# Performance work log

Hardware: AMD Instinct MI355X
Metric: run time of the kernel (lower is better)

## Reference

```python
import jax, jax.numpy as jnp
import numpy as np

B, T, I, H = 32, 2048, 256, 256
LN_EPS = 1e-5


def _lstm_dir(x, Wih, Whh, b):
    """Single-direction LSTM. x: [B,T,I]; Wih: [4H,I]; Whh: [4H,H]; b: [4H].
    PyTorch gate order: i, f, g, o. Returns hidden sequence [B,T,H]."""
    # Precompute input projection for all timesteps (one big GEMM).
    xW = jnp.einsum('bti,gi->btg', x, Wih) + b  # [B,T,4H]
    xW = jnp.swapaxes(xW, 0, 1)                 # [T,B,4H] for scan
    h0 = jnp.zeros((x.shape[0], Whh.shape[1]), x.dtype)
    c0 = jnp.zeros_like(h0)

    def step(carry, xt):
        h, c = carry
        gates = xt + h @ Whh.T                  # [B,4H]
        i, f, g, o = jnp.split(gates, 4, axis=-1)
        i = jax.nn.sigmoid(i)
        f = jax.nn.sigmoid(f)
        g = jnp.tanh(g)
        o = jax.nn.sigmoid(o)
        c = f * c + i * g
        h = o * jnp.tanh(c)
        return (h, c), h

    _, hs = jax.lax.scan(step, (h0, c0), xW)
    return jnp.swapaxes(hs, 0, 1)               # [B,T,H]


def _forward(x, Wih_f, Whh_f, b_f, Wih_b, Whh_b, b_b, ln_g, ln_b, fc_W, fc_b):
    h_fwd = _lstm_dir(x, Wih_f, Whh_f, b_f)
    h_bwd = _lstm_dir(x[:, ::-1, :], Wih_b, Whh_b, b_b)[:, ::-1, :]
    h = jnp.concatenate([h_fwd, h_bwd], axis=-1)     # [B,T,2H]
    # LayerNorm over last dim
    mu = jnp.mean(h, axis=-1, keepdims=True)
    var = jnp.mean((h - mu) ** 2, axis=-1, keepdims=True)
    h = (h - mu) * jax.lax.rsqrt(var + LN_EPS) * ln_g + ln_b
    # Linear 2H -> H (bidirectional branch). Dropout is identity in eval mode.
    return jnp.einsum('btk,hk->bth', h, fc_W) + fc_b


def setup_inputs() -> dict:
    key = jax.random.key(0)
    ks = jax.random.split(key, 10)
    s = 1.0 / np.sqrt(H)
    return {
        'x': jax.random.normal(ks[0], (B, T, I), jnp.float32),
        'Wih_f': jax.random.uniform(ks[1], (4 * H, I), jnp.float32, -s, s),
        'Whh_f': jax.random.uniform(ks[2], (4 * H, H), jnp.float32, -s, s),
        'b_f': jax.random.uniform(ks[3], (4 * H,), jnp.float32, -s, s),
        'Wih_b': jax.random.uniform(ks[4], (4 * H, I), jnp.float32, -s, s),
        'Whh_b': jax.random.uniform(ks[5], (4 * H, H), jnp.float32, -s, s),
        'b_b': jax.random.uniform(ks[6], (4 * H,), jnp.float32, -s, s),
        'ln_g': jnp.ones((2 * H,), jnp.float32),
        'ln_b': jnp.zeros((2 * H,), jnp.float32),
        'fc_W': jax.random.uniform(ks[7], (H, 2 * H), jnp.float32, -s, s),
        'fc_b': jax.random.uniform(ks[8], (H,), jnp.float32, -s, s),
    }


def reference(x, Wih_f, Whh_f, b_f, Wih_b, Whh_b, b_b, ln_g, ln_b, fc_W, fc_b):
    return _forward(x, Wih_f, Whh_f, b_f, Wih_b, Whh_b, b_b, ln_g, ln_b, fc_W, fc_b)
```

## Files before the change

kernel.cpp:

```cpp
#include <hip/hip_runtime.h>
#include <cstdint>
#include <cstddef>

#define BDIM 32
#define TDIM 2048
#define IDIM 256
#define HDIM 256
#define CHUNK 128
#define NCHUNK (TDIM / CHUNK)
#define GEMM_WGS 512

using short8 = __attribute__((ext_vector_type(8))) short;
using f32x4  = __attribute__((ext_vector_type(4))) float;
typedef _Float16 half2v __attribute__((ext_vector_type(2)));

__device__ __forceinline__ float bflo(uint32_t u) { return __uint_as_float(u << 16); }
__device__ __forceinline__ float bfhi(uint32_t u) { return __uint_as_float(u & 0xffff0000u); }
__device__ __forceinline__ uint16_t f2bf(float f) {
  uint32_t u = __float_as_uint(f);
  uint32_t r = u + 0x7fffu + ((u >> 16) & 1u);
  return (uint16_t)(r >> 16);
}
__device__ __forceinline__ uint16_t f2h_bits(float f) {
  _Float16 h = (_Float16)f;
  return __builtin_bit_cast(uint16_t, h);
}
__device__ __forceinline__ float h2f(uint16_t b) {
  return (float)__builtin_bit_cast(_Float16, b);
}
__device__ __forceinline__ half2v as_h2(uint32_t u) {
  return __builtin_bit_cast(half2v, u);
}
__device__ __forceinline__ float h2lo(uint32_t u) { return (float)as_h2(u)[0]; }
__device__ __forceinline__ float h2hi(uint32_t u) { return (float)as_h2(u)[1]; }

#if __has_builtin(__builtin_amdgcn_fdot2)
__device__ __forceinline__ float DOT2(half2v a, half2v b, float c) {
  return __builtin_amdgcn_fdot2(a, b, c, false);
}
#else
__device__ __forceinline__ float DOT2(half2v a, half2v b, float c) {
  return c + (float)a[0] * (float)b[0] + (float)a[1] * (float)b[1];
}
#endif

__device__ __forceinline__ float sigmoidf_fast(float x) {
  return 1.f / (1.f + __expf(-x));
}
__device__ __forceinline__ float tanhf_fast(float x) {
  float a = fabsf(x);
  float e = __expf(2.f * a);
  float t = 1.f - 2.f / (e + 1.f);
  return copysignf(t, x);
}


__global__ void k_cvt4(const float* __restrict__ src, uint16_t* __restrict__ dst, int n4) {
  int i = blockIdx.x * blockDim.x + threadIdx.x;
  if (i >= n4) return;
  const float4 v = ((const float4*)src)[i];
  ushort4 o;
  o.x = f2bf(v.x); o.y = f2bf(v.y); o.z = f2bf(v.z); o.w = f2bf(v.w);
  ((ushort4*)dst)[i] = o;
}

__global__ void k_zero(float* __restrict__ p, int n) {
  int i = blockIdx.x * blockDim.x + threadIdx.x;
  if (i < n) p[i] = 0.f;
}

__global__ void k_build_wcat(const float* __restrict__ wf, const float* __restrict__ wb,
                             const float* __restrict__ biasf, const float* __restrict__ biasb,
                             uint16_t* __restrict__ wcat, float* __restrict__ biasp) {
  int id = blockIdx.x * 256 + threadIdx.x;
  int k = id & 255;
  int j = id >> 8;
  int dir = j >> 10;
  int jj = j & 1023;
  int n = jj >> 2;
  int g = jj & 3;
  const float* W = dir ? wb : wf;
  wcat[id] = f2bf(W[(g * 256 + n) * 256 + k]);
  if (k == 0) biasp[j] = (dir ? biasb : biasf)[g * 256 + n];
}

__global__ void k_build_wrec2(const float* __restrict__ whf, const float* __restrict__ whb,
                              uint16_t* __restrict__ wrec2) {
  int id = blockIdx.x * 256 + threadIdx.x;
  int j  = id & 1;
  int g  = (id >> 1) & 3;
  int n  = (id >> 3) & 255;
  int kp = (id >> 11) & 127;
  int dir = (id >> 18) & 1;
  const float* W = dir ? whb : whf;
  wrec2[id] = f2h_bits(W[(g * 256 + n) * 256 + 2 * kp + j]);
}

__global__ __launch_bounds__(1024) void k_fused(
    const float* __restrict__ x,
    const uint16_t* __restrict__ wcat,
    const float* __restrict__ biasp,
    uint16_t* __restrict__ xw_prod,
    const uint16_t* __restrict__ xw_cons,
    const uint16_t* __restrict__ wrec2,
    uint16_t* __restrict__ hcat,
    float* __restrict__ hstate,
    float* __restrict__ cstate,
    int c0, int c0g, int do_lstm, int do_gemm) {
  const int tid = threadIdx.x;

  if (blockIdx.x < 64) {
    if (!do_lstm) return;
    __shared__ uint16_t hhalf[256];
    __shared__ float part[4][256][4];

    const int w = blockIdx.x;
    const int b = w >> 1;
    const int dir = w & 1;
    const int n = tid & 255;
    const int q = tid >> 8;

    const uint16_t* wbase = wrec2 + ((size_t)(dir * 128 + q * 32) * 256 + n) * 8;

    float c = 0.f, hlast = 0.f;
    if (tid < 256) {
      hlast = hstate[w * 256 + tid];
      c = cstate[w * 256 + tid];
      hhalf[tid] = f2h_bits(hlast);
    }
    __syncthreads();

    for (int sl = 0; sl < CHUNK; ++sl) {
      const int t = dir ? (TDIM - 1 - (c0 + sl)) : (c0 + sl);

      uint2 xv;
      if (tid < 256)
        xv = *(const uint2*)(xw_cons + ((size_t)(sl * 32 + b)) * 2048 + dir * 1024 + tid * 4);

      float ai = 0.f, af = 0.f, ag = 0.f, ao = 0.f;
      const uint16_t* wp = wbase;
#pragma unroll 8
      for (int it = 0; it < 32; ++it) {
        const half2v hp = as_h2(*(const uint32_t*)&hhalf[2 * (q * 32 + it)]);
        const uint4 wv = *(const uint4*)wp;
        wp += 2048;
        ai = DOT2(as_h2(wv.x), hp, ai);
        af = DOT2(as_h2(wv.y), hp, af);
        ag = DOT2(as_h2(wv.z), hp, ag);
        ao = DOT2(as_h2(wv.w), hp, ao);
      }
      f32x4 pv; pv[0] = ai; pv[1] = af; pv[2] = ag; pv[3] = ao;
      *(f32x4*)(&part[q][n][0]) = pv;
      __syncthreads();

      if (tid < 256) {
        const f32x4 p0 = *(const f32x4*)(&part[0][tid][0]);
        const f32x4 p1 = *(const f32x4*)(&part[1][tid][0]);
        const f32x4 p2 = *(const f32x4*)(&part[2][tid][0]);
        const f32x4 p3 = *(const f32x4*)(&part[3][tid][0]);
        float gi = p0[0] + p1[0] + p2[0] + p3[0] + h2lo(xv.x);
        float gf = p0[1] + p1[1] + p2[1] + p3[1] + h2hi(xv.x);
        float gg = p0[2] + p1[2] + p2[2] + p3[2] + h2lo(xv.y);
        float go = p0[3] + p1[3] + p2[3] + p3[3] + h2hi(xv.y);
        const float I = sigmoidf_fast(gi);
        const float F = sigmoidf_fast(gf);
        const float G = tanhf_fast(gg);
        const float O = sigmoidf_fast(go);
        c = F * c + I * G;
        const float h = O * tanhf_fast(c);
        hlast = h;
        const uint16_t hb = f2h_bits(h);
        hhalf[tid] = hb;
        hcat[((size_t)(b * TDIM + t)) * 512 + dir * 256 + tid] = hb;
      }
      __syncthreads();
    }

    if (tid < 256) {
      hstate[w * 256 + tid] = hlast;
      cstate[w * 256 + tid] = c;
    }
    return;
  }

  if (!do_gemm) return;
  const int gb = blockIdx.x - 64;
  const int mt = gb >> 4;
  const int nt = gb & 15;
  const int dir = nt >> 3;
  const int wv_ = tid >> 6;
  const int wm = wv_ & 3;
  const int wn = wv_ >> 2;
  const int lane = tid & 63;
  const int l15 = lane & 15;
  const int lg  = lane >> 4;

  const float* Abase[2];
  int colg[2];
  const uint16_t* Bbase[2];
  float bv[2], fvv[2];
#pragma unroll
  for (int mi = 0; mi < 2; ++mi) {
    const int row = mt * 128 + wm * 32 + mi * 16 + l15;
    const int s_local = row >> 5;
    const int b = row & 31;
    const int t = dir ? (TDIM - 1 - (c0g + s_local)) : (c0g + s_local);
    Abase[mi] = x + ((size_t)(b * TDIM + t)) * 256 + lg * 8;
  }
#pragma unroll
  for (int ni = 0; ni < 2; ++ni) {
    colg[ni] = nt * 128 + wn * 32 + ni * 16 + l15;
    Bbase[ni] = wcat + (size_t)colg[ni] * 256 + lg * 8;
    bv[ni] = biasp[colg[ni]];
    (void)fvv;
  }

  f32x4 acc[2][2] = {};
#pragma unroll
  for (int ks = 0; ks < 8; ++ks) {
    short8 a[2];
#pragma unroll
    for (int mi = 0; mi < 2; ++mi) {
      const float4 f0 = *(const float4*)(Abase[mi] + ks * 32);
      const float4 f1 = *(const float4*)(Abase[mi] + ks * 32 + 4);
      a[mi][0] = (short)f2bf(f0.x); a[mi][1] = (short)f2bf(f0.y);
      a[mi][2] = (short)f2bf(f0.z); a[mi][3] = (short)f2bf(f0.w);
      a[mi][4] = (short)f2bf(f1.x); a[mi][5] = (short)f2bf(f1.y);
      a[mi][6] = (short)f2bf(f1.z); a[mi][7] = (short)f2bf(f1.w);
    }
#pragma unroll
    for (int ni = 0; ni < 2; ++ni) {
      const short8 bfr = *(const short8*)(Bbase[ni] + ks * 32);
#pragma unroll
      for (int mi = 0; mi < 2; ++mi)
        acc[mi][ni] = __builtin_amdgcn_mfma_f32_16x16x32_bf16(a[mi], bfr, acc[mi][ni], 0, 0, 0);
    }
  }

#pragma unroll
  for (int mi = 0; mi < 2; ++mi)
#pragma unroll
    for (int ni = 0; ni < 2; ++ni)
#pragma unroll
      for (int r = 0; r < 4; ++r) {
        const int row = mt * 128 + wm * 32 + mi * 16 + lg * 4 + r;
        xw_prod[(size_t)row * 2048 + colg[ni]] = f2h_bits(acc[mi][ni][r] + bv[ni]);
      }
}

__global__ __launch_bounds__(256) void k_lnfc2(
    const uint16_t* __restrict__ hcat,
    const float* __restrict__ lng, const float* __restrict__ lnb,
    const uint16_t* __restrict__ fcwb,
    const float* __restrict__ fcb,
    float* __restrict__ out) {
  __shared__ uint16_t lnh[64 * 520];
  __shared__ float slng[512], slnb[512];

  const int tid = threadIdx.x;
  const size_t bt0 = (size_t)blockIdx.x * 64;

  slng[tid] = lng[tid]; slng[tid + 256] = lng[tid + 256];
  slnb[tid] = lnb[tid]; slnb[tid + 256] = lnb[tid + 256];

  const int row = tid >> 2;
  const int part = tid & 3;
  const uint16_t* hrow = hcat + (bt0 + row) * 512;
  float s = 0.f, s2 = 0.f;
#pragma unroll
  for (int i = 0; i < 16; ++i) {
    const uint4 u = *(const uint4*)(hrow + (i * 4 + part) * 8);
    const float f0 = h2lo(u.x), f1 = h2hi(u.x), f2 = h2lo(u.y), f3 = h2hi(u.y);
    const float f4 = h2lo(u.z), f5 = h2hi(u.z), f6 = h2lo(u.w), f7 = h2hi(u.w);
    s  += ((f0 + f1) + (f2 + f3)) + ((f4 + f5) + (f6 + f7));
    s2 += ((f0*f0 + f1*f1) + (f2*f2 + f3*f3)) + ((f4*f4 + f5*f5) + (f6*f6 + f7*f7));
  }
  s  += __shfl_xor(s, 1, 64);  s  += __shfl_xor(s, 2, 64);
  s2 += __shfl_xor(s2, 1, 64); s2 += __shfl_xor(s2, 2, 64);
  const float mu = s * (1.f / 512.f);
  const float var = s2 * (1.f / 512.f) - mu * mu;
  const float rs = rsqrtf(var + 1e-5f);
  __syncthreads();

#pragma unroll
  for (int i = 0; i < 16; ++i) {
    const int kb = (i * 4 + part) * 8;
    const uint4 u = *(const uint4*)(hrow + kb);
    uint16_t tmp[8] __attribute__((aligned(16)));
    const float f[8] = { h2lo(u.x), h2hi(u.x), h2lo(u.y), h2hi(u.y),
                         h2lo(u.z), h2hi(u.z), h2lo(u.w), h2hi(u.w) };
#pragma unroll
    for (int e = 0; e < 8; ++e)
      tmp[e] = f2bf((f[e] - mu) * rs * slng[kb + e] + slnb[kb + e]);
    *(short8*)&lnh[row * 520 + kb] = *(const short8*)tmp;
  }
  __syncthreads();

  const int w = tid >> 6;
  const int lane = tid & 63;
  const int l15 = lane & 15;
  const int lg = lane >> 4;
  f32x4 acc[4][4] = {};
#pragma unroll
  for (int nf = 0; nf < 4; ++nf) {
    const uint16_t* bb = fcwb + (size_t)(w * 64 + nf * 16 + l15) * 512 + lg * 8;
#pragma unroll 4
    for (int k0 = 0; k0 < 16; ++k0) {
      const short8 bfr = *(const short8*)(bb + k0 * 32);
#pragma unroll
      for (int mf = 0; mf < 4; ++mf) {
        const short8 afr = *(const short8*)&lnh[(mf * 16 + l15) * 520 + k0 * 32 + lg * 8];
        acc[mf][nf] = __builtin_amdgcn_mfma_f32_16x16x32_bf16(afr, bfr, acc[mf][nf], 0, 0, 0);
      }
    }
  }
#pragma unroll
  for (int nf = 0; nf < 4; ++nf) {
    const int col = w * 64 + nf * 16 + l15;
    const float fv = fcb[col];
#pragma unroll
    for (int mf = 0; mf < 4; ++mf)
#pragma unroll
      for (int r = 0; r < 4; ++r)
        out[(bt0 + mf * 16 + lg * 4 + r) * 256 + col] = acc[mf][nf][r] + fv;
  }
}


extern "C" void kernel_launch(void* const* d_in, const int* in_sizes, int n_in,
                              void* d_out, int out_size, void* d_ws, size_t ws_size,
                              hipStream_t stream) {
  const float* x    = (const float*)d_in[0];
  const float* Wihf = (const float*)d_in[1];
  const float* Whhf = (const float*)d_in[2];
  const float* bf_  = (const float*)d_in[3];
  const float* Wihb = (const float*)d_in[4];
  const float* Whhb = (const float*)d_in[5];
  const float* bb_  = (const float*)d_in[6];
  const float* lng  = (const float*)d_in[7];
  const float* lnb  = (const float*)d_in[8];
  const float* fcW  = (const float*)d_in[9];
  const float* fcb  = (const float*)d_in[10];
  float* out = (float*)d_out;

  char* ws = (char*)d_ws;
  size_t off = 0;
  uint16_t* wcat  = (uint16_t*)(ws + off); off += (size_t)2048 * 256 * 2;
  float*    biasp = (float*)(ws + off);    off += (size_t)2048 * 4;
  uint16_t* wrec2 = (uint16_t*)(ws + off); off += (size_t)2 * 128 * 256 * 8 * 2;
  uint16_t* fcwb  = (uint16_t*)(ws + off); off += (size_t)256 * 512 * 2;
  float*    hstate= (float*)(ws + off);    off += (size_t)64 * 256 * 4;
  float*    cstate= (float*)(ws + off);    off += (size_t)64 * 256 * 4;
  uint16_t* xw0   = (uint16_t*)(ws + off); off += (size_t)(CHUNK * 32) * 2048 * 2;
  uint16_t* xw1   = (uint16_t*)(ws + off); off += (size_t)(CHUNK * 32) * 2048 * 2;
  uint16_t* hcat  = (uint16_t*)(ws + off); off += (size_t)65536 * 512 * 2;
  (void)ws_size; (void)in_sizes; (void)n_in; (void)out_size;

  k_cvt4<<<128, 256, 0, stream>>>(fcW, fcwb, 131072 / 4);
  k_build_wcat<<<2048, 256, 0, stream>>>(Wihf, Wihb, bf_, bb_, wcat, biasp);
  k_build_wrec2<<<2048, 256, 0, stream>>>(Whhf, Whhb, wrec2);
  k_zero<<<128, 256, 0, stream>>>(hstate, 64 * 256 * 2);

  k_fused<<<64 + GEMM_WGS, 1024, 0, stream>>>(x, wcat, biasp, xw0, xw1, wrec2,
                                              hcat, hstate, cstate, 0, 0, 0, 1);

  for (int ck = 0; ck < NCHUNK; ++ck) {
    uint16_t* cons = (ck & 1) ? xw1 : xw0;
    uint16_t* prod = (ck & 1) ? xw0 : xw1;
    const int dg = (ck < NCHUNK - 1) ? 1 : 0;
    const int grid = 64 + (dg ? GEMM_WGS : 0);
    k_fused<<<grid, 1024, 0, stream>>>(x, wcat, biasp, prod, cons, wrec2,
                                       hcat, hstate, cstate,
                                       ck * CHUNK, (ck + 1) * CHUNK, 1, dg);
  }

  k_lnfc2<<<1024, 256, 0, stream>>>(hcat, lng, lnb, fcwb, fcb, out);
}
```

Baseline: 8.640 ms.

## Replace chunked LSTM launches with persistent cross-block kernel using register-resident weights

```diff
diff --git a/kernel.cpp b/kernel.cpp
--- a/kernel.cpp
+++ b/kernel.cpp
@@ -8,14 +8,11 @@
 #define HDIM 256
 #define CHUNK 128
 #define NCHUNK (TDIM / CHUNK)
-#define GEMM_WGS 512
 
 using short8 = __attribute__((ext_vector_type(8))) short;
 using f32x4  = __attribute__((ext_vector_type(4))) float;
 typedef _Float16 half2v __attribute__((ext_vector_type(2)));
 
-__device__ __forceinline__ float bflo(uint32_t u) { return __uint_as_float(u << 16); }
-__device__ __forceinline__ float bfhi(uint32_t u) { return __uint_as_float(u & 0xffff0000u); }
 __device__ __forceinline__ uint16_t f2bf(float f) {
   uint32_t u = __float_as_uint(f);
   uint32_t r = u + 0x7fffu + ((u >> 16) & 1u);
@@ -24,9 +21,6 @@
 __device__ __forceinline__ uint16_t f2h_bits(float f) {
   _Float16 h = (_Float16)f;
   return __builtin_bit_cast(uint16_t, h);
-}
-__device__ __forceinline__ float h2f(uint16_t b) {
-  return (float)__builtin_bit_cast(_Float16, b);
 }
 __device__ __forceinline__ half2v as_h2(uint32_t u) {
   return __builtin_bit_cast(half2v, u);
@@ -64,9 +58,9 @@
   ((ushort4*)dst)[i] = o;
 }
 
-__global__ void k_zero(float* __restrict__ p, int n) {
+__global__ void k_zero_u32(uint32_t* __restrict__ p, int n) {
   int i = blockIdx.x * blockDim.x + threadIdx.x;
-  if (i < n) p[i] = 0.f;
+  if (i < n) p[i] = 0u;
 }
 
 __global__ void k_build_wcat(const float* __restrict__ wf, const float* __restrict__ wb,
@@ -84,168 +78,191 @@
   if (k == 0) biasp[j] = (dir ? biasb : biasf)[g * 256 + n];
 }
 
-__global__ void k_build_wrec2(const float* __restrict__ whf, const float* __restrict__ whb,
-                              uint16_t* __restrict__ wrec2) {
+__global__ void k_build_wrec3(const float* __restrict__ whf, const float* __restrict__ whb,
+                              uint32_t* __restrict__ wrec3) {
   int id = blockIdx.x * 256 + threadIdx.x;
-  int j  = id & 1;
-  int g  = (id >> 1) & 3;
-  int n  = (id >> 3) & 255;
-  int kp = (id >> 11) & 127;
-  int dir = (id >> 18) & 1;
+  int g   = id & 3;
+  int n   = (id >> 2) & 63;
+  int j   = (id >> 8) & 15;
+  int kq  = (id >> 12) & 7;
+  int qq  = (id >> 15) & 3;
+  int dir = (id >> 17) & 1;
   const float* W = dir ? whb : whf;
-  wrec2[id] = f2h_bits(W[(g * 256 + n) * 256 + 2 * kp + j]);
-}
-
-__global__ __launch_bounds__(1024) void k_fused(
+  const int row = g * 256 + qq * 64 + n;
+  const int k0  = kq * 32 + 2 * j;
+  const uint32_t lo = f2h_bits(W[row * 256 + k0]);
+  const uint32_t hi = f2h_bits(W[row * 256 + k0 + 1]);
+  const int oidx = ((((dir * 4 + qq) * 8 + kq) * 16 + j) * 64 + n) * 4 + g;
+  wrec3[oidx] = lo | (hi << 16);
+}
+
+__global__ __launch_bounds__(512, 2) void k_lstm_persist(
     const float* __restrict__ x,
     const uint16_t* __restrict__ wcat,
     const float* __restrict__ biasp,
-    uint16_t* __restrict__ xw_prod,
-    const uint16_t* __restrict__ xw_cons,
-    const uint16_t* __restrict__ wrec2,
-    uint16_t* __restrict__ hcat,
-    float* __restrict__ hstate,
-    float* __restrict__ cstate,
-    int c0, int c0g, int do_lstm, int do_gemm) {
-  const int tid = threadIdx.x;
-
-  if (blockIdx.x < 64) {
-    if (!do_lstm) return;
-    __shared__ uint16_t hhalf[256];
-    __shared__ float part[4][256][4];
-
-    const int w = blockIdx.x;
-    const int b = w >> 1;
-    const int dir = w & 1;
-    const int n = tid & 255;
-    const int q = tid >> 8;
-
-    const uint16_t* wbase = wrec2 + ((size_t)(dir * 128 + q * 32) * 256 + n) * 8;
-
-    float c = 0.f, hlast = 0.f;
-    if (tid < 256) {
-      hlast = hstate[w * 256 + tid];
-      c = cstate[w * 256 + tid];
-      hhalf[tid] = f2h_bits(hlast);
+    const uint32_t* __restrict__ wrec3,
+    uint16_t* __restrict__ xwp_all,
+    uint32_t* __restrict__ hcat32,
+    uint32_t* __restrict__ cnt) {
+  __shared__ uint4 ldsbig[84 * 1024 / 16];
+  f32x4*    partsh = (f32x4*)ldsbig;
+  uint32_t* h2lds  = (uint32_t*)(ldsbig + 448);
+
+  const int bid  = blockIdx.x;
+  const int pair = bid & 63;
+  const int q    = bid >> 6;
+  const int b    = pair >> 1;
+  const int dir  = pair & 1;
+  const int tid  = threadIdx.x;
+  const int kq   = tid >> 6;
+  const int lane = tid & 63;
+
+  uint4 wr[16];
+  {
+    const uint4* wsrc = (const uint4*)wrec3 + ((((dir * 4 + q) * 8 + kq) * 16) * 64 + lane);
+#pragma unroll
+    for (int j = 0; j < 16; ++j) wr[j] = wsrc[j * 64];
+  }
+
+  if (tid < 128) h2lds[tid] = 0u;
+  float creg = 0.f;
+  __syncthreads();
+
+  uint16_t* xwp = xwp_all + (size_t)bid * (2 * CHUNK * 256);
+  const int l15 = lane & 15;
+  const int lg  = lane >> 4;
+  const int colbase = dir * 1024 + q * 256;
+  const uint32_t cmy = pair * 4 + q;
+
+  auto gemm_chunk = [&](int ck) {
+    const int p = ck & 1;
+    const int sl0 = kq * 16;
+    const int slA = sl0 + l15;
+    const int tA = dir ? (TDIM - 1 - (ck * CHUNK + slA)) : (ck * CHUNK + slA);
+    const float* Abase = x + ((size_t)(b * TDIM + tA)) * 256 + lg * 8;
+    uint16_t* xo = xwp + (size_t)p * (CHUNK * 256);
+#pragma unroll
+    for (int np = 0; np < 2; ++np) {
+      f32x4 acc[8] = {};
+#pragma unroll
+      for (int ks = 0; ks < 8; ++ks) {
+        const float4 f0 = *(const float4*)(Abase + ks * 32);
+        const float4 f1 = *(const float4*)(Abase + ks * 32 + 4);
+        short8 a;
+        a[0] = (short)f2bf(f0.x); a[1] = (short)f2bf(f0.y);
+        a[2] = (short)f2bf(f0.z); a[3] = (short)f2bf(f0.w);
+        a[4] = (short)f2bf(f1.x); a[5] = (short)f2bf(f1.y);
+        a[6] = (short)f2bf(f1.z); a[7] = (short)f2bf(f1.w);
+#pragma unroll
+        for (int nf = 0; nf < 8; ++nf) {
+          const uint16_t* Bp = wcat + (size_t)(colbase + np * 128 + nf * 16 + l15) * 256 + ks * 32 + lg * 8;
+          const short8 bfr = *(const short8*)Bp;
+          acc[nf] = __builtin_amdgcn_mfma_f32_16x16x32_bf16(a, bfr, acc[nf], 0, 0, 0);
+        }
+      }
+#pragma unroll
+      for (int nf = 0; nf < 8; ++nf) {
+        const int l = np * 128 + nf * 16 + l15;
+        const float bv = biasp[colbase + l];
+#pragma unroll
+        for (int r = 0; r < 4; ++r) {
+          const int row = sl0 + lg * 4 + r;
+          xo[row * 256 + l] = f2h_bits(acc[nf][r] + bv);
+        }
+      }
     }
-    __syncthreads();
+  };
+
+  gemm_chunk(0);
+
+  for (int ck = 0; ck < NCHUNK; ++ck) {
+    if (ck + 1 < NCHUNK) gemm_chunk(ck + 1);
+    const uint16_t* xin = xwp + (size_t)(ck & 1) * (CHUNK * 256);
 
     for (int sl = 0; sl < CHUNK; ++sl) {
-      const int t = dir ? (TDIM - 1 - (c0 + sl)) : (c0 + sl);
-
-      uint2 xv;
-      if (tid < 256)
-        xv = *(const uint2*)(xw_cons + ((size_t)(sl * 32 + b)) * 2048 + dir * 1024 + tid * 4);
-
+      const int s = ck * CHUNK + sl;
+      const int t = dir ? (TDIM - 1 - s) : s;
+
+      uint2 xv; xv.x = 0u; xv.y = 0u;
+      if (tid < 64) xv = *(const uint2*)(xin + sl * 256 + tid * 4);
+
+      const uint32_t h0 = h2lds[lane];
+      const uint32_t h1 = h2lds[64 + lane];
       float ai = 0.f, af = 0.f, ag = 0.f, ao = 0.f;
-      const uint16_t* wp = wbase;
-#pragma unroll 8
-      for (int it = 0; it < 32; ++it) {
-        const half2v hp = as_h2(*(const uint32_t*)&hhalf[2 * (q * 32 + it)]);
-        const uint4 wv = *(const uint4*)wp;
-        wp += 2048;
-        ai = DOT2(as_h2(wv.x), hp, ai);
-        af = DOT2(as_h2(wv.y), hp, af);
-        ag = DOT2(as_h2(wv.z), hp, ag);
-        ao = DOT2(as_h2(wv.w), hp, ao);
+      const int rb = (kq & 3) * 16;
+      if (kq < 4) {
+#pragma unroll
+        for (int j = 0; j < 16; ++j) {
+          const uint32_t hw = __builtin_amdgcn_readlane(h0, rb + j);
+          ai = DOT2(as_h2(wr[j].x), as_h2(hw), ai);
+          af = DOT2(as_h2(wr[j].y), as_h2(hw), af);
+          ag = DOT2(as_h2(wr[j].z), as_h2(hw), ag);
+          ao = DOT2(as_h2(wr[j].w), as_h2(hw), ao);
+        }
+      } else {
+#pragma unroll
+        for (int j = 0; j < 16; ++j) {
+          const uint32_t hw = __builtin_amdgcn_readlane(h1, rb + j);
+          ai = DOT2(as_h2(wr[j].x), as_h2(hw), ai);
+          af = DOT2(as_h2(wr[j].y), as_h2(hw), af);
+          ag = DOT2(as_h2(wr[j].z), as_h2(hw), ag);
+          ao = DOT2(as_h2(wr[j].w), as_h2(hw), ao);
+        }
       }
       f32x4 pv; pv[0] = ai; pv[1] = af; pv[2] = ag; pv[3] = ao;
-      *(f32x4*)(&part[q][n][0]) = pv;
+      if (kq > 0) partsh[(kq - 1) * 64 + lane] = pv;
       __syncthreads();
 
-      if (tid < 256) {
-        const f32x4 p0 = *(const f32x4*)(&part[0][tid][0]);
-        const f32x4 p1 = *(const f32x4*)(&part[1][tid][0]);
-        const f32x4 p2 = *(const f32x4*)(&part[2][tid][0]);
-        const f32x4 p3 = *(const f32x4*)(&part[3][tid][0]);
-        float gi = p0[0] + p1[0] + p2[0] + p3[0] + h2lo(xv.x);
-        float gf = p0[1] + p1[1] + p2[1] + p3[1] + h2hi(xv.x);
-        float gg = p0[2] + p1[2] + p2[2] + p3[2] + h2lo(xv.y);
-        float go = p0[3] + p1[3] + p2[3] + p3[3] + h2hi(xv.y);
+      const size_t rowbase = ((size_t)(b * TDIM + t)) * 256 + dir * 128;
+      if (tid < 64) {
+        f32x4 g = pv;
+#pragma unroll
+        for (int r = 0; r < 7; ++r) g += partsh[r * 64 + lane];
+        const float gi = g[0] + h2lo(xv.x);
+        const float gf = g[1] + h2hi(xv.x);
+        const float gg = g[2] + h2lo(xv.y);
+        const float go = g[3] + h2hi(xv.y);
         const float I = sigmoidf_fast(gi);
         const float F = sigmoidf_fast(gf);
         const float G = tanhf_fast(gg);
         const float O = sigmoidf_fast(go);
-        c = F * c + I * G;
-        const float h = O * tanhf_fast(c);
-        hlast = h;
-        const uint16_t hb = f2h_bits(h);
-        hhalf[tid] = hb;
-        hcat[((size_t)(b * TDIM + t)) * 512 + dir * 256 + tid] = hb;
+        creg = F * creg + I * G;
+        const float h = O * tanhf_fast(creg);
+        const uint32_t hb = (uint32_t)f2h_bits(h);
+        const uint32_t hp = (uint32_t)__shfl((int)hb, tid | 1, 64);
+        if ((tid & 1) == 0) {
+          const uint32_t hv = (hb & 0xffffu) | (hp << 16);
+          const int m = tid >> 1;
+          h2lds[q * 32 + m] = hv;
+          __hip_atomic_store(&hcat32[rowbase + q * 32 + m], hv,
+                             __ATOMIC_RELAXED, __HIP_MEMORY_SCOPE_AGENT);
+        }
       }
       __syncthreads();
+      if (tid == 0)
+        __hip_atomic_store(&cnt[cmy], (uint32_t)(s + 1),
+                           __ATOMIC_RELEASE, __HIP_MEMORY_SCOPE_AGENT);
+
+      if (s + 1 < TDIM) {
+        if (tid < 3) {
+          const int qo = tid + (tid >= q ? 1 : 0);
+          while (__hip_atomic_load(&cnt[pair * 4 + qo],
+                                   __ATOMIC_ACQUIRE, __HIP_MEMORY_SCOPE_AGENT) <= (uint32_t)s)
+            __builtin_amdgcn_s_sleep(2);
+        }
+        __syncthreads();
+        if (tid < 96) {
+          const int grp = tid >> 5;
+          const int qo = grp + (grp >= q ? 1 : 0);
+          const int ii = tid & 31;
+          const uint32_t hv = __hip_atomic_load(&hcat32[rowbase + qo * 32 + ii],
+                                                __ATOMIC_RELAXED, __HIP_MEMORY_SCOPE_AGENT);
+          h2lds[qo * 32 + ii] = hv;
+        }
+        __syncthreads();
+      }
     }
-
-    if (tid < 256) {
-      hstate[w * 256 + tid] = hlast;
-      cstate[w * 256 + tid] = c;
-    }
-    return;
-  }
-
-  if (!do_gemm) return;
-  const int gb = blockIdx.x - 64;
-  const int mt = gb >> 4;
-  const int nt = gb & 15;
-  const int dir = nt >> 3;
-  const int wv_ = tid >> 6;
-  const int wm = wv_ & 3;
-  const int wn = wv_ >> 2;
-  const int lane = tid & 63;
-  const int l15 = lane & 15;
-  const int lg  = lane >> 4;
-
-  const float* Abase[2];
-  int colg[2];
-  const uint16_t* Bbase[2];
-  float bv[2], fvv[2];
-#pragma unroll
-  for (int mi = 0; mi < 2; ++mi) {
-    const int row = mt * 128 + wm * 32 + mi * 16 + l15;
-    const int s_local = row >> 5;
-    const int b = row & 31;
-    const int t = dir ? (TDIM - 1 - (c0g + s_local)) : (c0g + s_local);
-    Abase[mi] = x + ((size_t)(b * TDIM + t)) * 256 + lg * 8;
-  }
-#pragma unroll
-  for (int ni = 0; ni < 2; ++ni) {
-    colg[ni] = nt * 128 + wn * 32 + ni * 16 + l15;
-    Bbase[ni] = wcat + (size_t)colg[ni] * 256 + lg * 8;
-    bv[ni] = biasp[colg[ni]];
-    (void)fvv;
-  }
-
-  f32x4 acc[2][2] = {};
-#pragma unroll
-  for (int ks = 0; ks < 8; ++ks) {
-    short8 a[2];
-#pragma unroll
-    for (int mi = 0; mi < 2; ++mi) {
-      const float4 f0 = *(const float4*)(Abase[mi] + ks * 32);
-      const float4 f1 = *(const float4*)(Abase[mi] + ks * 32 + 4);
-      a[mi][0] = (short)f2bf(f0.x); a[mi][1] = (short)f2bf(f0.y);
-      a[mi][2] = (short)f2bf(f0.z); a[mi][3] = (short)f2bf(f0.w);
-      a[mi][4] = (short)f2bf(f1.x); a[mi][5] = (short)f2bf(f1.y);
-      a[mi][6] = (short)f2bf(f1.z); a[mi][7] = (short)f2bf(f1.w);
-    }
-#pragma unroll
-    for (int ni = 0; ni < 2; ++ni) {
-      const short8 bfr = *(const short8*)(Bbase[ni] + ks * 32);
-#pragma unroll
-      for (int mi = 0; mi < 2; ++mi)
-        acc[mi][ni] = __builtin_amdgcn_mfma_f32_16x16x32_bf16(a[mi], bfr, acc[mi][ni], 0, 0, 0);
-    }
-  }
-
-#pragma unroll
-  for (int mi = 0; mi < 2; ++mi)
-#pragma unroll
-    for (int ni = 0; ni < 2; ++ni)
-#pragma unroll
-      for (int r = 0; r < 4; ++r) {
-        const int row = mt * 128 + wm * 32 + mi * 16 + lg * 4 + r;
-        xw_prod[(size_t)row * 2048 + colg[ni]] = f2h_bits(acc[mi][ni][r] + bv[ni]);
-      }
+  }
 }
 
 __global__ __launch_bounds__(256) void k_lnfc2(
@@ -347,32 +364,20 @@
   size_t off = 0;
   uint16_t* wcat  = (uint16_t*)(ws + off); off += (size_t)2048 * 256 * 2;
   float*    biasp = (float*)(ws + off);    off += (size_t)2048 * 4;
-  uint16_t* wrec2 = (uint16_t*)(ws + off); off += (size_t)2 * 128 * 256 * 8 * 2;
+  uint32_t* wrec3 = (uint32_t*)(ws + off); off += (size_t)262144 * 4;
   uint16_t* fcwb  = (uint16_t*)(ws + off); off += (size_t)256 * 512 * 2;
-  float*    hstate= (float*)(ws + off);    off += (size_t)64 * 256 * 4;
-  float*    cstate= (float*)(ws + off);    off += (size_t)64 * 256 * 4;
-  uint16_t* xw0   = (uint16_t*)(ws + off); off += (size_t)(CHUNK * 32) * 2048 * 2;
-  uint16_t* xw1   = (uint16_t*)(ws + off); off += (size_t)(CHUNK * 32) * 2048 * 2;
+  uint32_t* cnt   = (uint32_t*)(ws + off); off += 4096;
+  uint16_t* xwp   = (uint16_t*)(ws + off); off += (size_t)256 * 2 * CHUNK * 256 * 2;
   uint16_t* hcat  = (uint16_t*)(ws + off); off += (size_t)65536 * 512 * 2;
   (void)ws_size; (void)in_sizes; (void)n_in; (void)out_size;
 
   k_cvt4<<<128, 256, 0, stream>>>(fcW, fcwb, 131072 / 4);
   k_build_wcat<<<2048, 256, 0, stream>>>(Wihf, Wihb, bf_, bb_, wcat, biasp);
-  k_build_wrec2<<<2048, 256, 0, stream>>>(Whhf, Whhb, wrec2);
-  k_zero<<<128, 256, 0, stream>>>(hstate, 64 * 256 * 2);
-
-  k_fused<<<64 + GEMM_WGS, 1024, 0, stream>>>(x, wcat, biasp, xw0, xw1, wrec2,
-                                              hcat, hstate, cstate, 0, 0, 0, 1);
-
-  for (int ck = 0; ck < NCHUNK; ++ck) {
-    uint16_t* cons = (ck & 1) ? xw1 : xw0;
-    uint16_t* prod = (ck & 1) ? xw0 : xw1;
-    const int dg = (ck < NCHUNK - 1) ? 1 : 0;
-    const int grid = 64 + (dg ? GEMM_WGS : 0);
-    k_fused<<<grid, 1024, 0, stream>>>(x, wcat, biasp, prod, cons, wrec2,
-                                       hcat, hstate, cstate,
-                                       ck * CHUNK, (ck + 1) * CHUNK, 1, dg);
-  }
+  k_build_wrec3<<<1024, 256, 0, stream>>>(Whhf, Whhb, wrec3);
+  k_zero_u32<<<1, 256, 0, stream>>>(cnt, 256);
+
+  k_lstm_persist<<<256, 512, 0, stream>>>(x, wcat, biasp, wrec3, xwp,
+                                          (uint32_t*)hcat, cnt);
 
   k_lnfc2<<<1024, 256, 0, stream>>>(hcat, lng, lnb, fcwb, fcb, out);
 }
```

Result: slower. 11.35 ms (+31.4%).
